# Kernel tuning notes

Measured on AMD Instinct MI355X. Metric: run time of the kernel, lower is better.

Reference implementation:

```python
import jax, jax.numpy as jnp
import numpy as np

B, PAD_LEN, HID, NB, NY = 1024, 127, 512, 128, 8
IN_DIM = 5 * (PAD_LEN + 1)          # LSTMCell input_size = 5*(pad_len+1)
MAX_TRIP, MAX_ROW = 10, 8
BARGE_PAR_WIDTH = 10.0


def setup_inputs() -> dict:
    key = jax.random.key(0)
    ks = jax.random.split(key, 12)
    s = 1.0 / np.sqrt(HID).astype(np.float32)
    return {
        "x": jax.random.normal(ks[0], (B, IN_DIM), jnp.float32),
        "h0": jnp.zeros((B, HID), jnp.float32),
        "c0": jnp.zeros((B, HID), jnp.float32),
        "W_ih": jax.random.normal(ks[1], (4 * HID, IN_DIM), jnp.float32) * s,
        "W_hh": jax.random.normal(ks[2], (4 * HID, HID), jnp.float32) * s,
        "b_ih": jax.random.normal(ks[3], (4 * HID,), jnp.float32) * s,
        "b_hh": jax.random.normal(ks[4], (4 * HID,), jnp.float32) * s,
        "W_fc": jax.random.normal(ks[5], (NB * NY, HID), jnp.float32) * s,
        "b_fc": jax.random.normal(ks[6], (NB * NY,), jnp.float32) * s,
        "block_size": jax.random.uniform(ks[7], (B, NB, 5), jnp.float32),
        "block_lengths_on_barge": jax.random.uniform(ks[8], (B, NY, MAX_TRIP, MAX_ROW), jnp.float32),
        "block_width_on_barge": jax.random.uniform(ks[9], (B, NY, MAX_TRIP, MAX_ROW), jnp.float32),
        "encoder_mask": jax.random.bernoulli(ks[10], 0.5, (B, NB, NY, PAD_LEN)),
        "block_mask": jnp.zeros((B, NB), bool),
        "barge_count": jax.random.randint(ks[11], (B, NY), 0, MAX_TRIP, jnp.int32),
        "barge_slot": -jnp.ones((B, NY, MAX_TRIP, MAX_ROW, 2), jnp.int32),
    }


def reference(x, h0, c0, W_ih, W_hh, b_ih, b_hh, W_fc, b_fc,
              block_size, block_lengths_on_barge, block_width_on_barge,
              encoder_mask, block_mask, barge_count, barge_slot):
    # ---- LSTMCell step (torch gate order: i, f, g, o) ----
    gates = x @ W_ih.T + b_ih + h0 @ W_hh.T + b_hh          # (B, 4H)
    i, f, g, o = jnp.split(gates, 4, axis=-1)
    c = jax.nn.sigmoid(f) * c0 + jax.nn.sigmoid(i) * jnp.tanh(g)
    h = jax.nn.sigmoid(o) * jnp.tanh(c)

    # ---- fc + masked softmax over (block, yard) joint actions ----
    logits = h @ W_fc.T + b_fc                               # (B, NB*NY)
    yard_feasible = jnp.any(encoder_mask, axis=-1)           # (B, NB, NY): block fits in some slot of yard
    valid = yard_feasible & (~block_mask)[:, :, None]        # unselected blocks only
    neg = jnp.asarray(-1e9, logits.dtype)
    probs = jax.nn.softmax(jnp.where(valid.reshape(valid.shape[0], -1), logits, neg), axis=-1)

    # ---- action decode + per-sample barge-slot scatter allocation ----
    Bsz = x.shape[0]
    bidx = jnp.arange(Bsz)
    action = jnp.argmax(probs, axis=-1)                      # greedy selection
    block_sel = action // NY
    yard_sel = (action % NY).astype(barge_count.dtype)
    cur = barge_count[bidx, yard_sel]                        # (B,) current barge idx per sample
    blen = block_size[bidx, block_sel, 0]                    # (B,)
    bwid = block_size[bidx, block_sel, 1]                    # (B,)

    widths = block_width_on_barge[bidx, yard_sel, cur]       # (B, MAX_ROW) gathered rows
    lens = block_lengths_on_barge[bidx, yard_sel, cur]       # (B, MAX_ROW)
    par_ok = widths <= BARGE_PAR_WIDTH                       # parallel-space feasibility per slot
    cand = jnp.where(par_ok, lens, -1.0)                     # invalid slots -> -1 (as in source)
    slot = jnp.argmax(cand, axis=-1)                         # best existing-length parallel slot

    barge_slot_new = barge_slot.at[bidx, yard_sel, cur, slot, 1].set(block_sel.astype(barge_slot.dtype))
    widths_new = block_width_on_barge.at[bidx, yard_sel, cur, slot].add(bwid)
    lengths_new = block_lengths_on_barge.at[bidx, yard_sel, cur, slot].max(blen)
    return probs, barge_slot_new, lengths_new, widths_new
```

## Files before the change

kernel.cpp:

```cpp
#include <hip/hip_runtime.h>
#include <math.h>

#define Bsz 1024
#define PADL 127
#define HID 512
#define NBb 128
#define NYd 8
#define INDIM 640
#define MTRIP 10
#define MROW 8
#define NBNY 1024
#define FOURH 2048
#define KCAT 1152

typedef short  bf16x8 __attribute__((ext_vector_type(8)));
typedef float  f32x4  __attribute__((ext_vector_type(4)));
typedef unsigned short u16x8 __attribute__((ext_vector_type(8)));

__device__ __forceinline__ float sigf(float x){ return 1.0f/(1.0f+expf(-x)); }

__device__ __forceinline__ unsigned short bf16rn(float x){
    unsigned int u = __float_as_uint(x);
    unsigned int r = (u + 0x7FFFu + ((u>>16)&1u)) >> 16;
    return (unsigned short)r;
}

__global__ __launch_bounds__(256) void convert_concat(
    const float* __restrict__ src1, const float* __restrict__ src2,
    unsigned short* __restrict__ dstH, unsigned short* __restrict__ dstL)
{
    int t = blockIdx.x*256 + threadIdx.x;
    int r  = t / 144;
    int c8 = t - r*144;
    const float* p = (c8 < 80) ? (src1 + (size_t)r*INDIM + c8*8)
                               : (src2 + (size_t)r*HID + (c8-80)*8);
    float4 v0 = *(const float4*)p;
    float4 v1 = *(const float4*)(p+4);
    float v[8] = {v0.x,v0.y,v0.z,v0.w,v1.x,v1.y,v1.z,v1.w};
    u16x8 hv, lv;
    #pragma unroll
    for (int i=0;i<8;++i){
        unsigned short h = bf16rn(v[i]);
        float hf = __uint_as_float(((unsigned int)h)<<16);
        unsigned short l = bf16rn(v[i]-hf);
        hv[i] = h; lv[i] = l;
    }
    size_t base = (size_t)r*KCAT + c8*8;
    *(u16x8*)(dstH + base) = hv;
    *(u16x8*)(dstL + base) = lv;
}

__global__ __launch_bounds__(256) void gemm_gates_mfma(
    const unsigned short* __restrict__ Ah_g, const unsigned short* __restrict__ Al_g,
    const unsigned short* __restrict__ Bh_g, const unsigned short* __restrict__ Bl_g,
    const float* __restrict__ bih, const float* __restrict__ bhh,
    float* __restrict__ gates)
{
    __shared__ __align__(16) unsigned short Ah_s[128*32];
    __shared__ __align__(16) unsigned short Al_s[128*32];
    __shared__ __align__(16) unsigned short Bh_s[64*32];
    __shared__ __align__(16) unsigned short Bl_s[64*32];

    const int t = threadIdx.x;
    const int lane = t & 63;
    const int w = t >> 6;
    const int wr = w >> 1, wc = w & 1;
    const int m0 = blockIdx.y*128, n0 = blockIdx.x*64;

    const int fa0 = t*8;
    const int fa1 = (256+t)*8;
    const int fb  = t*8;
    const int ar0 = fa0>>5, ac0 = fa0&31;
    const int ar1 = fa1>>5, ac1 = fa1&31;
    const int brow = fb>>5, bcol = fb&31;

    f32x4 acc[4][2];
    #pragma unroll
    for (int m=0;m<4;++m){
        #pragma unroll
        for (int n=0;n<2;++n) acc[m][n] = (f32x4){0.f,0.f,0.f,0.f};
    }

    uint4 rah0, rah1, ral0, ral1, rbh, rbl;
    auto load6 = [&](int k0){
        rah0 = *(const uint4*)(Ah_g + (size_t)(m0+ar0)*KCAT + k0 + ac0);
        rah1 = *(const uint4*)(Ah_g + (size_t)(m0+ar1)*KCAT + k0 + ac1);
        ral0 = *(const uint4*)(Al_g + (size_t)(m0+ar0)*KCAT + k0 + ac0);
        ral1 = *(const uint4*)(Al_g + (size_t)(m0+ar1)*KCAT + k0 + ac1);
        rbh  = *(const uint4*)(Bh_g + (size_t)(n0+brow)*KCAT + k0 + bcol);
        rbl  = *(const uint4*)(Bl_g + (size_t)(n0+brow)*KCAT + k0 + bcol);
    };

    load6(0);
    for (int s=0; s<KCAT/32; ++s){
        __syncthreads();
        *(uint4*)&Ah_s[fa0] = rah0;  *(uint4*)&Ah_s[fa1] = rah1;
        *(uint4*)&Al_s[fa0] = ral0;  *(uint4*)&Al_s[fa1] = ral1;
        *(uint4*)&Bh_s[fb]  = rbh;   *(uint4*)&Bl_s[fb]  = rbl;
        __syncthreads();
        if (s+1 < KCAT/32) load6((s+1)*32);

        const int kc = (lane>>4)*8;
        bf16x8 afh[4], afl[4], bfh[2], bfl[2];
        #pragma unroll
        for (int m=0;m<4;++m){
            int idx = (wr*64 + m*16 + (lane&15))*32 + kc;
            afh[m] = *(const bf16x8*)&Ah_s[idx];
            afl[m] = *(const bf16x8*)&Al_s[idx];
        }
        #pragma unroll
        for (int n=0;n<2;++n){
            int idx = (wc*32 + n*16 + (lane&15))*32 + kc;
            bfh[n] = *(const bf16x8*)&Bh_s[idx];
            bfl[n] = *(const bf16x8*)&Bl_s[idx];
        }
        #pragma unroll
        for (int m=0;m<4;++m){
            #pragma unroll
            for (int n=0;n<2;++n){
                acc[m][n] = __builtin_amdgcn_mfma_f32_16x16x32_bf16(afh[m], bfh[n], acc[m][n], 0,0,0);
                acc[m][n] = __builtin_amdgcn_mfma_f32_16x16x32_bf16(afh[m], bfl[n], acc[m][n], 0,0,0);
                acc[m][n] = __builtin_amdgcn_mfma_f32_16x16x32_bf16(afl[m], bfh[n], acc[m][n], 0,0,0);
            }
        }
    }

    #pragma unroll
    for (int m=0;m<4;++m){
        #pragma unroll
        for (int n=0;n<2;++n){
            int row = m0 + wr*64 + m*16 + ((lane>>4)<<2);
            int col = n0 + wc*32 + n*16 + (lane&15);
            float bsum = bih[col] + bhh[col];
            #pragma unroll
            for (int q=0;q<4;++q)
                gates[(size_t)(row+q)*FOURH + col] = acc[m][n][q] + bsum;
        }
    }
}

__global__ __launch_bounds__(256) void gemm_fc_f32(
    const float* __restrict__ A, const float* __restrict__ B,
    const float* __restrict__ bias, float* __restrict__ C)
{
    __shared__ float As[2][16][68];
    __shared__ float Bs[2][16][68];
    const int tid = threadIdx.x;
    const int m0 = blockIdx.y*64, n0 = blockIdx.x*64;
    const int lr = tid>>2, lc = (tid&3)*4;
    const int tm = (tid>>4)*4, tn = (tid&15)*4;
    float acc[4][4] = {{0,0,0,0},{0,0,0,0},{0,0,0,0},{0,0,0,0}};

    float4 pa, pb;
    auto prefetch = [&](int k0){
        pa = *(const float4*)(A + (size_t)(m0+lr)*HID + k0 + lc);
        pb = *(const float4*)(B + (size_t)(n0+lr)*HID + k0 + lc);
    };
    auto stage = [&](int buf){
        As[buf][lc+0][lr]=pa.x; As[buf][lc+1][lr]=pa.y;
        As[buf][lc+2][lr]=pa.z; As[buf][lc+3][lr]=pa.w;
        Bs[buf][lc+0][lr]=pb.x; Bs[buf][lc+1][lr]=pb.y;
        Bs[buf][lc+2][lr]=pb.z; Bs[buf][lc+3][lr]=pb.w;
    };

    prefetch(0); stage(0); __syncthreads();
    int buf = 0;
    for (int s=0; s<HID/16; ++s){
        if (s+1 < HID/16) prefetch((s+1)*16);
        #pragma unroll
        for (int kk=0; kk<16; ++kk){
            float4 a = *(const float4*)&As[buf][kk][tm];
            float4 b = *(const float4*)&Bs[buf][kk][tn];
            float a4[4]={a.x,a.y,a.z,a.w}, b4[4]={b.x,b.y,b.z,b.w};
            #pragma unroll
            for (int i=0;i<4;i++)
                #pragma unroll
                for (int j=0;j<4;j++) acc[i][j] += a4[i]*b4[j];
        }
        if (s+1 < HID/16){ stage(buf^1); __syncthreads(); buf ^= 1; }
    }
    #pragma unroll
    for (int i=0;i<4;i++){
        int row = m0+tm+i;
        #pragma unroll
        for (int j=0;j<4;j++){
            int col = n0+tn+j;
            C[(size_t)row*NBNY + col] = acc[i][j] + bias[col];
        }
    }
}

__global__ __launch_bounds__(256) void lstm_kernel(const float* __restrict__ gates,
    const float* __restrict__ c0, float* __restrict__ h)
{
    int idx = blockIdx.x*256 + threadIdx.x;
    int b = idx >> 7, j4 = (idx & 127)*4;
    const float* g = gates + (size_t)b*FOURH;
    float4 iv = *(const float4*)(g + j4);
    float4 fv = *(const float4*)(g + 512 + j4);
    float4 gv = *(const float4*)(g + 1024 + j4);
    float4 ov = *(const float4*)(g + 1536 + j4);
    float4 cv = *(const float4*)(c0 + (size_t)b*HID + j4);
    float4 hv;
    hv.x = sigf(ov.x)*tanhf(sigf(fv.x)*cv.x + sigf(iv.x)*tanhf(gv.x));
    hv.y = sigf(ov.y)*tanhf(sigf(fv.y)*cv.y + sigf(iv.y)*tanhf(gv.y));
    hv.z = sigf(ov.z)*tanhf(sigf(fv.z)*cv.z + sigf(iv.z)*tanhf(gv.z));
    hv.w = sigf(ov.w)*tanhf(sigf(fv.w)*cv.w + sigf(iv.w)*tanhf(gv.w));
    *(float4*)(h + (size_t)b*HID + j4) = hv;
}

__device__ __forceinline__ int row_any(const int* __restrict__ p){
    #pragma unroll 1
    for (int j=0; j<124; j+=4){
        if (p[j] | p[j+1] | p[j+2] | p[j+3]) return 1;
    }
    return (p[124] | p[125] | p[126]) ? 1 : 0;
}

__global__ __launch_bounds__(256) void softmax_fused(
    const float* __restrict__ logits, const int* __restrict__ em,
    const int* __restrict__ bmask, const int* __restrict__ bcount,
    const float* __restrict__ bsize, const float* __restrict__ bwid_in,
    const float* __restrict__ blen_in,
    float* __restrict__ probs,
    int* __restrict__ pslot, int* __restrict__ pblock,
    float* __restrict__ pblen, float* __restrict__ pbwid)
{
    int b = blockIdx.x, t = threadIdx.x;
    __shared__ float red[256];
    __shared__ int  redi[256];
    const float* lrow = logits + (size_t)b*NBNY;

    float ml[4]; float mymax = -INFINITY;
    #pragma unroll
    for (int r=0;r<4;++r){
        int c = t + r*256;
        int nb = c >> 3;
        int v = 0;
        if (bmask[b*NBb + nb] == 0)
            v = row_any(em + (size_t)(b*NBNY + c)*PADL);
        float m = v ? lrow[c] : -1e9f;
        ml[r] = m; mymax = fmaxf(mymax, m);
    }
    red[t]=mymax; __syncthreads();
    for (int s=128;s>0;s>>=1){ if(t<s) red[t]=fmaxf(red[t],red[t+s]); __syncthreads(); }
    float rowmax = red[0]; __syncthreads();

    float p[4]; float mysum=0.f;
    #pragma unroll
    for (int r=0;r<4;++r){ p[r]=expf(ml[r]-rowmax); mysum+=p[r]; }
    red[t]=mysum; __syncthreads();
    for (int s=128;s>0;s>>=1){ if(t<s) red[t]+=red[t+s]; __syncthreads(); }
    float inv = 1.0f/red[0]; __syncthreads();

    float bv=-INFINITY; int bi=0;
    #pragma unroll
    for (int r=0;r<4;++r){
        int c = t + r*256;
        float pr = p[r]*inv;
        probs[(size_t)b*NBNY + c] = pr;
        if (pr > bv){ bv=pr; bi=c; }
    }
    red[t]=bv; redi[t]=bi; __syncthreads();
    for (int s=128;s>0;s>>=1){
        if (t<s){
            float ov=red[t+s]; int oi=redi[t+s];
            if (ov>red[t] || (ov==red[t] && oi<redi[t])){ red[t]=ov; redi[t]=oi; }
        }
        __syncthreads();
    }

    if (t==0){
        int a = redi[0];
        int blk = a / NYd, yard = a % NYd;
        int cur = bcount[b*NYd + yard];
        int base = ((b*NYd + yard)*MTRIP + cur)*MROW;
        float bestv = -INFINITY; int bests = 0;
        #pragma unroll
        for (int s=0;s<MROW;++s){
            float w = bwid_in[base+s];
            float l = blen_in[base+s];
            float cand = (w <= 10.0f) ? l : -1.0f;
            if (cand > bestv){ bestv=cand; bests=s; }
        }
        pslot[b]  = base + bests;
        pblock[b] = blk;
        pblen[b]  = bsize[(b*NBb + blk)*5 + 0];
        pbwid[b]  = bsize[(b*NBb + blk)*5 + 1];
    }
}

__global__ __launch_bounds__(256) void finalize_kernel(const int* __restrict__ bslot,
    const float* __restrict__ blen_in, const float* __restrict__ bwid_in,
    const int* __restrict__ pslot, const int* __restrict__ pblock,
    const float* __restrict__ pblen, const float* __restrict__ pbwid,
    float* __restrict__ out_slot, float* __restrict__ out_len, float* __restrict__ out_wid)
{
    int i = blockIdx.x*256 + threadIdx.x;
    if (i < Bsz*NYd*MTRIP*MROW*2){
        int b = i / (NYd*MTRIP*MROW*2);
        float v = (float)bslot[i];
        if (i == pslot[b]*2 + 1) v = (float)pblock[b];
        out_slot[i] = v;
    }
    if (i < Bsz*NYd*MTRIP*MROW){
        int b = i / (NYd*MTRIP*MROW);
        float l = blen_in[i], w = bwid_in[i];
        if (i == pslot[b]){ l = fmaxf(l, pblen[b]); w = w + pbwid[b]; }
        out_len[i] = l;
        out_wid[i] = w;
    }
}

extern "C" void kernel_launch(void* const* d_in, const int* in_sizes, int n_in,
                              void* d_out, int out_size, void* d_ws, size_t ws_size,
                              hipStream_t stream)
{
    const float* x    = (const float*)d_in[0];
    const float* h0   = (const float*)d_in[1];
    const float* c0   = (const float*)d_in[2];
    const float* Wih  = (const float*)d_in[3];
    const float* Whh  = (const float*)d_in[4];
    const float* bih  = (const float*)d_in[5];
    const float* bhh  = (const float*)d_in[6];
    const float* Wfc  = (const float*)d_in[7];
    const float* bfc  = (const float*)d_in[8];
    const float* bsize= (const float*)d_in[9];
    const float* blen = (const float*)d_in[10];
    const float* bwid = (const float*)d_in[11];
    const int*   em   = (const int*)d_in[12];
    const int*   bmask= (const int*)d_in[13];
    const int*   bcount=(const int*)d_in[14];
    const int*   bslot= (const int*)d_in[15];

    float* out      = (float*)d_out;
    float* probs    = out;
    float* out_slot = out + 1048576;
    float* out_len  = out + 1048576 + 1310720;
    float* out_wid  = out_len + 655360;

    float* ws     = (float*)d_ws;
    float* gates  = ws;
    float* h      = ws + 2097152;
    float* logits = ws + 2621440;
    unsigned short* Ah = (unsigned short*)(ws + 3670016);
    unsigned short* Al = (unsigned short*)(ws + 4259840);
    unsigned short* Bh = (unsigned short*)(ws + 4849664);
    unsigned short* Bl = (unsigned short*)(ws + 6029312);
    int*   pslot  = (int*)(ws + 7208960);
    int*   pblock = (int*)(ws + 7209984);
    float* pblen  = ws + 7211008;
    float* pbwid  = ws + 7212032;

    convert_concat<<<576, 256, 0, stream>>>(x, h0, Ah, Al);
    convert_concat<<<1152, 256, 0, stream>>>(Wih, Whh, Bh, Bl);
    gemm_gates_mfma<<<dim3(FOURH/64, Bsz/128), 256, 0, stream>>>(
        Ah, Al, Bh, Bl, bih, bhh, gates);
    lstm_kernel<<<512, 256, 0, stream>>>(gates, c0, h);
    gemm_fc_f32<<<dim3(NBNY/64, Bsz/64), 256, 0, stream>>>(h, Wfc, bfc, logits);
    softmax_fused<<<Bsz, 256, 0, stream>>>(logits, em, bmask, bcount, bsize, bwid, blen,
                                           probs, pslot, pblock, pblen, pbwid);
    finalize_kernel<<<5120, 256, 0, stream>>>(bslot, blen, bwid, pslot, pblock, pblen, pbwid,
                                              out_slot, out_len, out_wid);
}
```

Baseline: 730.9 us.

## Replace fp32 FC GEMM with 3-way split bf16 MFMA GEMM and merge conversions

The fc GEMM from h to logits moves from scalar fp32 FMA to bf16 MFMA instructions. Near-fp32 accuracy is kept by splitting both h and W_fc into three bf16 parts and summing six cross-product MFMAs per tile. The LSTM kernel now writes h directly as three bf16 parts. All fp32-to-bf16 conversions (x/h0, W_ih/W_hh, W_fc) are merged into one launch. This trades more MFMA work and extra conversion traffic for much higher matrix throughput, with some risk of small numerical differences.

```diff
diff --git a/kernel.cpp b/kernel.cpp
--- a/kernel.cpp
+++ b/kernel.cpp
@@ -16,6 +16,7 @@
 typedef short  bf16x8 __attribute__((ext_vector_type(8)));
 typedef float  f32x4  __attribute__((ext_vector_type(4)));
 typedef unsigned short u16x8 __attribute__((ext_vector_type(8)));
+typedef unsigned short u16x4 __attribute__((ext_vector_type(4)));
 
 __device__ __forceinline__ float sigf(float x){ return 1.0f/(1.0f+expf(-x)); }
 
@@ -24,30 +25,65 @@
     unsigned int r = (u + 0x7FFFu + ((u>>16)&1u)) >> 16;
     return (unsigned short)r;
 }
-
-__global__ __launch_bounds__(256) void convert_concat(
-    const float* __restrict__ src1, const float* __restrict__ src2,
-    unsigned short* __restrict__ dstH, unsigned short* __restrict__ dstL)
-{
-    int t = blockIdx.x*256 + threadIdx.x;
-    int r  = t / 144;
-    int c8 = t - r*144;
-    const float* p = (c8 < 80) ? (src1 + (size_t)r*INDIM + c8*8)
-                               : (src2 + (size_t)r*HID + (c8-80)*8);
-    float4 v0 = *(const float4*)p;
-    float4 v1 = *(const float4*)(p+4);
-    float v[8] = {v0.x,v0.y,v0.z,v0.w,v1.x,v1.y,v1.z,v1.w};
-    u16x8 hv, lv;
-    #pragma unroll
-    for (int i=0;i<8;++i){
-        unsigned short h = bf16rn(v[i]);
-        float hf = __uint_as_float(((unsigned int)h)<<16);
-        unsigned short l = bf16rn(v[i]-hf);
-        hv[i] = h; lv[i] = l;
-    }
-    size_t base = (size_t)r*KCAT + c8*8;
-    *(u16x8*)(dstH + base) = hv;
-    *(u16x8*)(dstL + base) = lv;
+__device__ __forceinline__ float bf2f(unsigned short h){
+    return __uint_as_float(((unsigned int)h)<<16);
+}
+
+__global__ __launch_bounds__(256) void convert_all(
+    const float* __restrict__ x,   const float* __restrict__ h0,
+    const float* __restrict__ Wih, const float* __restrict__ Whh,
+    const float* __restrict__ Wfc,
+    unsigned short* __restrict__ Ah, unsigned short* __restrict__ Al,
+    unsigned short* __restrict__ Bh, unsigned short* __restrict__ Bl,
+    unsigned short* __restrict__ W1, unsigned short* __restrict__ W2,
+    unsigned short* __restrict__ W3)
+{
+    int blk = blockIdx.x;
+    if (blk < 1728){
+        const float* s1; const float* s2;
+        unsigned short* dH; unsigned short* dL;
+        int t;
+        if (blk < 576){ s1=x; s2=h0; dH=Ah; dL=Al; t = blk*256 + threadIdx.x; }
+        else          { s1=Wih; s2=Whh; dH=Bh; dL=Bl; t = (blk-576)*256 + threadIdx.x; }
+        int r  = t / 144;
+        int c8 = t - r*144;
+        const float* p = (c8 < 80) ? (s1 + (size_t)r*INDIM + c8*8)
+                                   : (s2 + (size_t)r*HID + (c8-80)*8);
+        float4 v0 = *(const float4*)p;
+        float4 v1 = *(const float4*)(p+4);
+        float v[8] = {v0.x,v0.y,v0.z,v0.w,v1.x,v1.y,v1.z,v1.w};
+        u16x8 hv, lv;
+        #pragma unroll
+        for (int i=0;i<8;++i){
+            unsigned short h = bf16rn(v[i]);
+            unsigned short l = bf16rn(v[i]-bf2f(h));
+            hv[i] = h; lv[i] = l;
+        }
+        size_t base = (size_t)r*KCAT + c8*8;
+        *(u16x8*)(dH + base) = hv;
+        *(u16x8*)(dL + base) = lv;
+    } else {
+        int t = (blk-1728)*256 + threadIdx.x;
+        int r  = t >> 6;
+        int c8 = t & 63;
+        const float* p = Wfc + (size_t)r*HID + c8*8;
+        float4 v0 = *(const float4*)p;
+        float4 v1 = *(const float4*)(p+4);
+        float v[8] = {v0.x,v0.y,v0.z,v0.w,v1.x,v1.y,v1.z,v1.w};
+        u16x8 w1, w2, w3;
+        #pragma unroll
+        for (int i=0;i<8;++i){
+            unsigned short a1 = bf16rn(v[i]);
+            float r1 = v[i] - bf2f(a1);
+            unsigned short a2 = bf16rn(r1);
+            unsigned short a3 = bf16rn(r1 - bf2f(a2));
+            w1[i]=a1; w2[i]=a2; w3[i]=a3;
+        }
+        size_t base = (size_t)r*HID + c8*8;
+        *(u16x8*)(W1 + base) = w1;
+        *(u16x8*)(W2 + base) = w2;
+        *(u16x8*)(W3 + base) = w3;
+    }
 }
 
 __global__ __launch_bounds__(256) void gemm_gates_mfma(
@@ -139,59 +175,10 @@
     }
 }
 
-__global__ __launch_bounds__(256) void gemm_fc_f32(
-    const float* __restrict__ A, const float* __restrict__ B,
-    const float* __restrict__ bias, float* __restrict__ C)
-{
-    __shared__ float As[2][16][68];
-    __shared__ float Bs[2][16][68];
-    const int tid = threadIdx.x;
-    const int m0 = blockIdx.y*64, n0 = blockIdx.x*64;
-    const int lr = tid>>2, lc = (tid&3)*4;
-    const int tm = (tid>>4)*4, tn = (tid&15)*4;
-    float acc[4][4] = {{0,0,0,0},{0,0,0,0},{0,0,0,0},{0,0,0,0}};
-
-    float4 pa, pb;
-    auto prefetch = [&](int k0){
-        pa = *(const float4*)(A + (size_t)(m0+lr)*HID + k0 + lc);
-        pb = *(const float4*)(B + (size_t)(n0+lr)*HID + k0 + lc);
-    };
-    auto stage = [&](int buf){
-        As[buf][lc+0][lr]=pa.x; As[buf][lc+1][lr]=pa.y;
-        As[buf][lc+2][lr]=pa.z; As[buf][lc+3][lr]=pa.w;
-        Bs[buf][lc+0][lr]=pb.x; Bs[buf][lc+1][lr]=pb.y;
-        Bs[buf][lc+2][lr]=pb.z; Bs[buf][lc+3][lr]=pb.w;
-    };
-
-    prefetch(0); stage(0); __syncthreads();
-    int buf = 0;
-    for (int s=0; s<HID/16; ++s){
-        if (s+1 < HID/16) prefetch((s+1)*16);
-        #pragma unroll
-        for (int kk=0; kk<16; ++kk){
-            float4 a = *(const float4*)&As[buf][kk][tm];
-            float4 b = *(const float4*)&Bs[buf][kk][tn];
-            float a4[4]={a.x,a.y,a.z,a.w}, b4[4]={b.x,b.y,b.z,b.w};
-            #pragma unroll
-            for (int i=0;i<4;i++)
-                #pragma unroll
-                for (int j=0;j<4;j++) acc[i][j] += a4[i]*b4[j];
-        }
-        if (s+1 < HID/16){ stage(buf^1); __syncthreads(); buf ^= 1; }
-    }
-    #pragma unroll
-    for (int i=0;i<4;i++){
-        int row = m0+tm+i;
-        #pragma unroll
-        for (int j=0;j<4;j++){
-            int col = n0+tn+j;
-            C[(size_t)row*NBNY + col] = acc[i][j] + bias[col];
-        }
-    }
-}
-
 __global__ __launch_bounds__(256) void lstm_kernel(const float* __restrict__ gates,
-    const float* __restrict__ c0, float* __restrict__ h)
+    const float* __restrict__ c0,
+    unsigned short* __restrict__ h1, unsigned short* __restrict__ h2,
+    unsigned short* __restrict__ h3)
 {
     int idx = blockIdx.x*256 + threadIdx.x;
     int b = idx >> 7, j4 = (idx & 127)*4;
@@ -201,12 +188,112 @@
     float4 gv = *(const float4*)(g + 1024 + j4);
     float4 ov = *(const float4*)(g + 1536 + j4);
     float4 cv = *(const float4*)(c0 + (size_t)b*HID + j4);
-    float4 hv;
-    hv.x = sigf(ov.x)*tanhf(sigf(fv.x)*cv.x + sigf(iv.x)*tanhf(gv.x));
-    hv.y = sigf(ov.y)*tanhf(sigf(fv.y)*cv.y + sigf(iv.y)*tanhf(gv.y));
-    hv.z = sigf(ov.z)*tanhf(sigf(fv.z)*cv.z + sigf(iv.z)*tanhf(gv.z));
-    hv.w = sigf(ov.w)*tanhf(sigf(fv.w)*cv.w + sigf(iv.w)*tanhf(gv.w));
-    *(float4*)(h + (size_t)b*HID + j4) = hv;
+    float hv[4];
+    hv[0] = sigf(ov.x)*tanhf(sigf(fv.x)*cv.x + sigf(iv.x)*tanhf(gv.x));
+    hv[1] = sigf(ov.y)*tanhf(sigf(fv.y)*cv.y + sigf(iv.y)*tanhf(gv.y));
+    hv[2] = sigf(ov.z)*tanhf(sigf(fv.z)*cv.z + sigf(iv.z)*tanhf(gv.z));
+    hv[3] = sigf(ov.w)*tanhf(sigf(fv.w)*cv.w + sigf(iv.w)*tanhf(gv.w));
+    u16x4 o1, o2, o3;
+    #pragma unroll
+    for (int i=0;i<4;++i){
+        unsigned short a1 = bf16rn(hv[i]);
+        float r1 = hv[i] - bf2f(a1);
+        unsigned short a2 = bf16rn(r1);
+        unsigned short a3 = bf16rn(r1 - bf2f(a2));
+        o1[i]=a1; o2[i]=a2; o3[i]=a3;
+    }
+    size_t base = (size_t)b*HID + j4;
+    *(u16x4*)(h1 + base) = o1;
+    *(u16x4*)(h2 + base) = o2;
+    *(u16x4*)(h3 + base) = o3;
+}
+
+__global__ __launch_bounds__(256) void gemm_fc_mfma(
+    const unsigned short* __restrict__ A1, const unsigned short* __restrict__ A2,
+    const unsigned short* __restrict__ A3,
+    const unsigned short* __restrict__ B1, const unsigned short* __restrict__ B2,
+    const unsigned short* __restrict__ B3,
+    const float* __restrict__ bfc, float* __restrict__ logits)
+{
+    __shared__ __align__(16) unsigned short As[3][64*32];
+    __shared__ __align__(16) unsigned short Bs[3][64*32];
+
+    const int t = threadIdx.x;
+    const int lane = t & 63;
+    const int w = t >> 6;
+    const int wr = w >> 1, wc = w & 1;
+    const int m0 = blockIdx.y*64, n0 = blockIdx.x*64;
+
+    const int fr = (t*8)>>5, fcol = (t*8)&31;
+
+    f32x4 acc[2][2];
+    #pragma unroll
+    for (int m=0;m<2;++m){
+        #pragma unroll
+        for (int n=0;n<2;++n) acc[m][n] = (f32x4){0.f,0.f,0.f,0.f};
+    }
+
+    uint4 ra1, ra2, ra3, rb1, rb2, rb3;
+    auto load6 = [&](int k0){
+        size_t aoff = (size_t)(m0+fr)*HID + k0 + fcol;
+        size_t boff = (size_t)(n0+fr)*HID + k0 + fcol;
+        ra1 = *(const uint4*)(A1 + aoff);
+        ra2 = *(const uint4*)(A2 + aoff);
+        ra3 = *(const uint4*)(A3 + aoff);
+        rb1 = *(const uint4*)(B1 + boff);
+        rb2 = *(const uint4*)(B2 + boff);
+        rb3 = *(const uint4*)(B3 + boff);
+    };
+
+    load6(0);
+    const int fa = t*8;
+    for (int s=0; s<HID/32; ++s){
+        __syncthreads();
+        *(uint4*)&As[0][fa] = ra1;  *(uint4*)&As[1][fa] = ra2;  *(uint4*)&As[2][fa] = ra3;
+        *(uint4*)&Bs[0][fa] = rb1;  *(uint4*)&Bs[1][fa] = rb2;  *(uint4*)&Bs[2][fa] = rb3;
+        __syncthreads();
+        if (s+1 < HID/32) load6((s+1)*32);
+
+        const int kc = (lane>>4)*8;
+        bf16x8 af[3][2], bf[3][2];
+        #pragma unroll
+        for (int m=0;m<2;++m){
+            int idx = (wr*32 + m*16 + (lane&15))*32 + kc;
+            #pragma unroll
+            for (int p=0;p<3;++p) af[p][m] = *(const bf16x8*)&As[p][idx];
+        }
+        #pragma unroll
+        for (int n=0;n<2;++n){
+            int idx = (wc*32 + n*16 + (lane&15))*32 + kc;
+            #pragma unroll
+            for (int p=0;p<3;++p) bf[p][n] = *(const bf16x8*)&Bs[p][idx];
+        }
+        #pragma unroll
+        for (int m=0;m<2;++m){
+            #pragma unroll
+            for (int n=0;n<2;++n){
+                acc[m][n] = __builtin_amdgcn_mfma_f32_16x16x32_bf16(af[0][m], bf[0][n], acc[m][n], 0,0,0);
+                acc[m][n] = __builtin_amdgcn_mfma_f32_16x16x32_bf16(af[0][m], bf[1][n], acc[m][n], 0,0,0);
+                acc[m][n] = __builtin_amdgcn_mfma_f32_16x16x32_bf16(af[1][m], bf[0][n], acc[m][n], 0,0,0);
+                acc[m][n] = __builtin_amdgcn_mfma_f32_16x16x32_bf16(af[0][m], bf[2][n], acc[m][n], 0,0,0);
+                acc[m][n] = __builtin_amdgcn_mfma_f32_16x16x32_bf16(af[1][m], bf[1][n], acc[m][n], 0,0,0);
+                acc[m][n] = __builtin_amdgcn_mfma_f32_16x16x32_bf16(af[2][m], bf[0][n], acc[m][n], 0,0,0);
+            }
+        }
+    }
+
+    #pragma unroll
+    for (int m=0;m<2;++m){
+        #pragma unroll
+        for (int n=0;n<2;++n){
+            int row = m0 + wr*32 + m*16 + ((lane>>4)<<2);
+            int col = n0 + wc*32 + n*16 + (lane&15);
+            float bsum = bfc[col];
+            #pragma unroll
+            for (int q=0;q<4;++q)
+                logits[(size_t)(row+q)*NBNY + col] = acc[m][n][q] + bsum;
+        }
+    }
 }
 
 __device__ __forceinline__ int row_any(const int* __restrict__ p){
@@ -339,25 +426,31 @@
     float* out_len  = out + 1048576 + 1310720;
     float* out_wid  = out_len + 655360;
 
-    float* ws     = (float*)d_ws;
+    float* ws = (float*)d_ws;
     float* gates  = ws;
-    float* h      = ws + 2097152;
-    float* logits = ws + 2621440;
-    unsigned short* Ah = (unsigned short*)(ws + 3670016);
-    unsigned short* Al = (unsigned short*)(ws + 4259840);
-    unsigned short* Bh = (unsigned short*)(ws + 4849664);
-    unsigned short* Bl = (unsigned short*)(ws + 6029312);
-    int*   pslot  = (int*)(ws + 7208960);
-    int*   pblock = (int*)(ws + 7209984);
-    float* pblen  = ws + 7211008;
-    float* pbwid  = ws + 7212032;
-
-    convert_concat<<<576, 256, 0, stream>>>(x, h0, Ah, Al);
-    convert_concat<<<1152, 256, 0, stream>>>(Wih, Whh, Bh, Bl);
+    float* logits = ws + 2097152;
+    unsigned short* Ah = (unsigned short*)(ws + 3145728);
+    unsigned short* Al = (unsigned short*)(ws + 3735552);
+    unsigned short* Bh = (unsigned short*)(ws + 4325376);
+    unsigned short* Bl = (unsigned short*)(ws + 5505024);
+    unsigned short* h1 = (unsigned short*)(ws + 6684672);
+    unsigned short* h2 = (unsigned short*)(ws + 6946816);
+    unsigned short* h3 = (unsigned short*)(ws + 7208960);
+    unsigned short* W1 = (unsigned short*)(ws + 7471104);
+    unsigned short* W2 = (unsigned short*)(ws + 7733248);
+    unsigned short* W3 = (unsigned short*)(ws + 7995392);
+    int*   pslot  = (int*)(ws + 8257536);
+    int*   pblock = (int*)(ws + 8258560);
+    float* pblen  = ws + 8259584;
+    float* pbwid  = ws + 8260608;
+
+    convert_all<<<1984, 256, 0, stream>>>(x, h0, Wih, Whh, Wfc,
+                                          Ah, Al, Bh, Bl, W1, W2, W3);
     gemm_gates_mfma<<<dim3(FOURH/64, Bsz/128), 256, 0, stream>>>(
         Ah, Al, Bh, Bl, bih, bhh, gates);
-    lstm_kernel<<<512, 256, 0, stream>>>(gates, c0, h);
-    gemm_fc_f32<<<dim3(NBNY/64, Bsz/64), 256, 0, stream>>>(h, Wfc, bfc, logits);
+    lstm_kernel<<<512, 256, 0, stream>>>(gates, c0, h1, h2, h3);
+    gemm_fc_mfma<<<dim3(NBNY/64, Bsz/64), 256, 0, stream>>>(
+        h1, h2, h3, W1, W2, W3, bfc, logits);
     softmax_fused<<<Bsz, 256, 0, stream>>>(logits, em, bmask, bcount, bsize, bwid, blen,
                                            probs, pslot, pblock, pblen, pbwid);
     finalize_kernel<<<5120, 256, 0, stream>>>(bslot, blen, bwid, pslot, pblock, pblen, pbwid,
```

New measurement: 720.2 us. No clear change (-1.5%).
